# Kernel optimization log

Hardware: AMD Instinct MI355X
Metric: run time of the kernel (lower is better)

## Reference

```python
import jax, jax.numpy as jnp
import numpy as np

N_NODES = 100000
N_EDGES = 600000
HIDDEN = 128
LN_EPS = 1e-8


def setup_inputs() -> dict:
    key = jax.random.key(0)
    k1, k2, k3 = jax.random.split(key, 3)
    x = jax.random.normal(k1, (N_NODES, HIDDEN), dtype=jnp.float32)
    edge_index = jax.random.randint(k2, (2, N_EDGES), 0, N_NODES, dtype=jnp.int32)
    # GCNConv linear weight (glorot-ish scale) and bias
    W = jax.random.normal(k3, (HIDDEN, HIDDEN), dtype=jnp.float32) / np.sqrt(HIDDEN)
    b = jnp.zeros((HIDDEN,), dtype=jnp.float32)
    ln_gamma = jnp.ones((HIDDEN,), dtype=jnp.float32)
    ln_beta = jnp.zeros((HIDDEN,), dtype=jnp.float32)
    return {"x": x, "edge_index": edge_index, "W": W, "b": b,
            "ln_gamma": ln_gamma, "ln_beta": ln_beta}


def _gcn_layer(x, edge_index, W, b, ln_gamma, ln_beta):
    n = x.shape[0]
    # --- GCNConv (PyG semantics): add self-loops, sym-normalize, x@W, scatter ---
    loop = jnp.arange(n, dtype=edge_index.dtype)
    src = jnp.concatenate([edge_index[0], loop])  # [E+N]
    dst = jnp.concatenate([edge_index[1], loop])
    deg = jax.ops.segment_sum(jnp.ones_like(dst, dtype=x.dtype), dst,
                              num_segments=n)  # in-degree incl. self-loop
    dinv = jnp.where(deg > 0, jax.lax.rsqrt(deg), 0.0)
    norm = dinv[src] * dinv[dst]  # [E+N]
    h = x @ W  # [N, H]
    msg = h[src] * norm[:, None]  # gather + scale, [E+N, H]
    agg = jax.ops.segment_sum(msg, dst, num_segments=n) + b  # scatter-sum
    # --- ReLU -> (dropout = identity in eval) -> residual -> LayerNorm ---
    y = jax.nn.relu(agg) + x
    mu = jnp.mean(y, axis=-1, keepdims=True)
    var = jnp.mean(jnp.square(y - mu), axis=-1, keepdims=True)
    return (y - mu) * jax.lax.rsqrt(var + LN_EPS) * ln_gamma + ln_beta


def reference(x, edge_index, W, b, ln_gamma, ln_beta):
    return _gcn_layer(x, edge_index, W, b, ln_gamma, ln_beta)
```

## Files before the change

### kernel.cpp

```cpp
#include <hip/hip_runtime.h>

#define HID 128
#define CAP 32
#define BM 64
#define EUN 8

typedef unsigned short u16;
typedef unsigned int u32;
typedef __attribute__((ext_vector_type(8))) short short8v;
typedef __attribute__((ext_vector_type(4))) float f32x4;
typedef __attribute__((ext_vector_type(4))) u32 u32x4;

__device__ inline u16 f2bf(float f) {
    union { float f; u32 u; } c; c.f = f;
    u32 u = c.u;
    return (u16)((u + 0x7FFFu + ((u >> 16) & 1u)) >> 16);
}
__device__ inline u32 pack2(float lo, float hi) {
    return (u32)f2bf(lo) | ((u32)f2bf(hi) << 16);
}
__device__ inline float bflo(u32 u) {
    union { u32 u; float f; } c; c.u = u << 16; return c.f;
}
__device__ inline float bfhi(u32 u) {
    union { u32 u; float f; } c; c.u = u & 0xFFFF0000u; return c.f;
}
__device__ inline float bf2f(u16 b) {
    union { u32 u; float f; } c; c.u = ((u32)b) << 16; return c.f;
}

__global__ __launch_bounds__(256) void k_countfill(const int* __restrict__ src,
                                                   const int* __restrict__ dst,
                                                   int* __restrict__ cnt,
                                                   int* __restrict__ csr, int e) {
    const int base = blockIdx.x * (256 * EUN) + threadIdx.x;
    int d[EUN], s[EUN], slot[EUN];
    #pragma unroll
    for (int u = 0; u < EUN; ++u) {
        int i = base + u * 256;
        if (i < e) {
            d[u] = __builtin_nontemporal_load(&dst[i]);
            s[u] = __builtin_nontemporal_load(&src[i]);
        }
    }
    #pragma unroll
    for (int u = 0; u < EUN; ++u)
        if (base + u * 256 < e) slot[u] = atomicAdd(&cnt[d[u]], 1);
    #pragma unroll
    for (int u = 0; u < EUN; ++u)
        if (base + u * 256 < e && slot[u] < CAP)
            csr[(size_t)d[u] * CAP + slot[u]] = s[u];
}

__global__ __launch_bounds__(256) void k_prep(const float* __restrict__ x,
                                              u16* __restrict__ xbf,
                                              const float* __restrict__ W,
                                              u16* __restrict__ wswz, int n) {
    int t = blockIdx.x * blockDim.x + threadIdx.x;
    if (t < n * 16) {
        int g = t >> 4, l = t & 15;
        const float4* p = (const float4*)&x[(size_t)g * HID + l * 8];
        float4 v0 = p[0], v1 = p[1];
        uint4 o;
        o.x = pack2(v0.x, v0.y);
        o.y = pack2(v0.z, v0.w);
        o.z = pack2(v1.x, v1.y);
        o.w = pack2(v1.z, v1.w);
        *(uint4*)&xbf[(size_t)g * HID + l * 8] = o;
    }
    if (t < 128 * 128) {
        int i = t & 7;
        int lane = (t >> 3) & 63;
        int ct = (t >> 9) & 7;
        int ks = t >> 12;
        int k = ks * 32 + (lane >> 4) * 8 + i;
        int col = ct * 16 + (lane & 15);
        wswz[t] = f2bf(W[k * HID + col]);
    }
}

__global__ __launch_bounds__(256) void k_fused(const u16* __restrict__ xbf,
                                               const int* __restrict__ cnt,
                                               const int* __restrict__ csr,
                                               const u16* __restrict__ wswz,
                                               const float* __restrict__ bvec,
                                               const float* __restrict__ gamma,
                                               const float* __restrict__ beta,
                                               float* __restrict__ out, int n) {
    __shared__ uint4 lds4[1024];
    char* lds = (char*)lds4;
    const int tid = threadIdx.x;
    const int row0 = blockIdx.x * BM;

    {
        const int grp = tid >> 4;
        const int l16 = tid & 15;
        const int j8 = l16 * 8;
        #pragma unroll
        for (int k = 0; k < 4; ++k) {
            int r = grp * 4 + k;
            int g = row0 + r;
            uint4 pk = make_uint4(0, 0, 0, 0);
            if (g < n) {
                const int len = min(cnt[g], CAP);
                const float dd = rsqrtf((float)(cnt[g] + 1));
                float acc[8];
                {
                    float s2 = dd * dd;
                    u32x4 hv = *(const u32x4*)&xbf[(size_t)g * HID + j8];
                    acc[0] = bflo(hv.x) * s2; acc[1] = bfhi(hv.x) * s2;
                    acc[2] = bflo(hv.y) * s2; acc[3] = bfhi(hv.y) * s2;
                    acc[4] = bflo(hv.z) * s2; acc[5] = bfhi(hv.z) * s2;
                    acc[6] = bflo(hv.w) * s2; acc[7] = bfhi(hv.w) * s2;
                }
                const size_t off = (size_t)g * CAP;
                for (int base = 0; base < len; base += 16) {
                    int idx = base + l16;
                    int sk = csr[off + (idx < len ? idx : 0)];
                    float dv = (idx < len) ? rsqrtf((float)(cnt[sk] + 1)) : 0.f;
                    int mm = (min(16, len - base) + 3) & ~3;
                    for (int j = 0; j < mm; j += 4) {
                        int s0 = __shfl(sk, j + 0, 16);
                        int s1 = __shfl(sk, j + 1, 16);
                        int s2 = __shfl(sk, j + 2, 16);
                        int s3 = __shfl(sk, j + 3, 16);
                        float w0 = __shfl(dv, j + 0, 16) * dd;
                        float w1 = __shfl(dv, j + 1, 16) * dd;
                        float w2 = __shfl(dv, j + 2, 16) * dd;
                        float w3 = __shfl(dv, j + 3, 16) * dd;
                        u32x4 h0 = *(const u32x4*)&xbf[(size_t)s0 * HID + j8];
                        u32x4 h1 = *(const u32x4*)&xbf[(size_t)s1 * HID + j8];
                        u32x4 h2 = *(const u32x4*)&xbf[(size_t)s2 * HID + j8];
                        u32x4 h3 = *(const u32x4*)&xbf[(size_t)s3 * HID + j8];
                        acc[0] = fmaf(bflo(h0.x), w0, acc[0]); acc[1] = fmaf(bfhi(h0.x), w0, acc[1]);
                        acc[2] = fmaf(bflo(h0.y), w0, acc[2]); acc[3] = fmaf(bfhi(h0.y), w0, acc[3]);
                        acc[4] = fmaf(bflo(h0.z), w0, acc[4]); acc[5] = fmaf(bfhi(h0.z), w0, acc[5]);
                        acc[6] = fmaf(bflo(h0.w), w0, acc[6]); acc[7] = fmaf(bfhi(h0.w), w0, acc[7]);
                        acc[0] = fmaf(bflo(h1.x), w1, acc[0]); acc[1] = fmaf(bfhi(h1.x), w1, acc[1]);
                        acc[2] = fmaf(bflo(h1.y), w1, acc[2]); acc[3] = fmaf(bfhi(h1.y), w1, acc[3]);
                        acc[4] = fmaf(bflo(h1.z), w1, acc[4]); acc[5] = fmaf(bfhi(h1.z), w1, acc[5]);
                        acc[6] = fmaf(bflo(h1.w), w1, acc[6]); acc[7] = fmaf(bfhi(h1.w), w1, acc[7]);
                        acc[0] = fmaf(bflo(h2.x), w2, acc[0]); acc[1] = fmaf(bfhi(h2.x), w2, acc[1]);
                        acc[2] = fmaf(bflo(h2.y), w2, acc[2]); acc[3] = fmaf(bfhi(h2.y), w2, acc[3]);
                        acc[4] = fmaf(bflo(h2.z), w2, acc[4]); acc[5] = fmaf(bfhi(h2.z), w2, acc[5]);
                        acc[6] = fmaf(bflo(h2.w), w2, acc[6]); acc[7] = fmaf(bfhi(h2.w), w2, acc[7]);
                        acc[0] = fmaf(bflo(h3.x), w3, acc[0]); acc[1] = fmaf(bfhi(h3.x), w3, acc[1]);
                        acc[2] = fmaf(bflo(h3.y), w3, acc[2]); acc[3] = fmaf(bfhi(h3.y), w3, acc[3]);
                        acc[4] = fmaf(bflo(h3.z), w3, acc[4]); acc[5] = fmaf(bfhi(h3.z), w3, acc[5]);
                        acc[6] = fmaf(bflo(h3.w), w3, acc[6]); acc[7] = fmaf(bfhi(h3.w), w3, acc[7]);
                    }
                }
                pk.x = pack2(acc[0], acc[1]);
                pk.y = pack2(acc[2], acc[3]);
                pk.z = pack2(acc[4], acc[5]);
                pk.w = pack2(acc[6], acc[7]);
            }
            int byte = r * 256 + l16 * 16;
            byte ^= (r & 7) << 4;
            *(uint4*)(lds + byte) = pk;
        }
    }
    __syncthreads();

    const int w = tid >> 6;
    const int l = tid & 63;
    const int c15 = l & 15;
    const short8v* wfrag = (const short8v*)wswz;

    f32x4 acc[8];
    #pragma unroll
    for (int c = 0; c < 8; ++c) acc[c] = (f32x4){0.f, 0.f, 0.f, 0.f};

    #pragma unroll
    for (int ks = 0; ks < 4; ++ks) {
        int row = w * 16 + c15;
        int byte = row * 256 + ks * 64 + (l >> 4) * 16;
        byte ^= (row & 7) << 4;
        short8v a = *(const short8v*)(lds + byte);
        #pragma unroll
        for (int ct = 0; ct < 8; ++ct) {
            short8v b = wfrag[(ks * 8 + ct) * 64 + l];
            acc[ct] = __builtin_amdgcn_mfma_f32_16x16x32_bf16(a, b, acc[ct], 0, 0, 0);
        }
    }

    float bb[8], gg[8], bz[8];
    #pragma unroll
    for (int ct = 0; ct < 8; ++ct) {
        bb[ct] = bvec[ct * 16 + c15];
        gg[ct] = gamma[ct * 16 + c15];
        bz[ct] = beta[ct * 16 + c15];
    }
    #pragma unroll
    for (int j = 0; j < 4; ++j) {
        int gr = row0 + w * 16 + (l >> 4) * 4 + j;
        if (gr < n) {
            const u16* xr = xbf + (size_t)gr * HID + c15;
            float v[8];
            #pragma unroll
            for (int ct = 0; ct < 8; ++ct)
                v[ct] = fmaxf(acc[ct][j] + bb[ct], 0.f) + bf2f(xr[ct * 16]);
            float sum = 0.f;
            #pragma unroll
            for (int ct = 0; ct < 8; ++ct) sum += v[ct];
            #pragma unroll
            for (int o = 1; o < 16; o <<= 1) sum += __shfl_xor(sum, o, 16);
            float mu = sum * (1.0f / HID);
            float d[8], vs = 0.f;
            #pragma unroll
            for (int ct = 0; ct < 8; ++ct) { d[ct] = v[ct] - mu; vs = fmaf(d[ct], d[ct], vs); }
            #pragma unroll
            for (int o = 1; o < 16; o <<= 1) vs += __shfl_xor(vs, o, 16);
            float inv = rsqrtf(vs * (1.0f / HID) + 1e-8f);
            float* orow = out + (size_t)gr * HID + c15;
            #pragma unroll
            for (int ct = 0; ct < 8; ++ct)
                __builtin_nontemporal_store(fmaf(d[ct] * inv, gg[ct], bz[ct]), &orow[ct * 16]);
        }
    }
}

extern "C" void kernel_launch(void* const* d_in, const int* in_sizes, int n_in,
                              void* d_out, int out_size, void* d_ws, size_t ws_size,
                              hipStream_t stream) {
    const float* x     = (const float*)d_in[0];
    const int*   ei    = (const int*)d_in[1];
    const float* W     = (const float*)d_in[2];
    const float* b     = (const float*)d_in[3];
    const float* gamma = (const float*)d_in[4];
    const float* beta  = (const float*)d_in[5];
    float* out = (float*)d_out;

    const int n = in_sizes[0] / HID;
    const int e = in_sizes[1] / 2;
    const int* src = ei;
    const int* dst = ei + e;

    u16* xbf  = (u16*)d_ws;
    int* cnt  = (int*)(xbf + (size_t)n * HID);
    int* csr  = cnt + n;
    u16* wswz = (u16*)(csr + (size_t)n * CAP);

    hipMemsetAsync(cnt, 0, (size_t)n * sizeof(int), stream);
    k_countfill<<<(e + 256 * EUN - 1) / (256 * EUN), 256, 0, stream>>>(src, dst, cnt, csr, e);
    k_prep<<<((size_t)n * 16 + 255) / 256, 256, 0, stream>>>(x, xbf, W, wswz, n);
    k_fused<<<(n + BM - 1) / BM, 256, 0, stream>>>(
        xbf, cnt, csr, wswz, b, gamma, beta, out, n);
}
```

Measured before the change: 102.3 us.

## Gather neighbor features as pre-scaled FP8 rows instead of bf16

The prep kernel now also writes a copy of x in FP8, with each row already scaled by its source-side degree normalisation, plus a zeroed sentinel row at index n. The aggregation loop gathers 128-byte FP8 rows instead of 256-byte bf16 rows. It no longer needs the per-neighbour count load and rsqrt, and it applies the destination scale once at the end. This halves the bandwidth of the random-access gather, at the cost of FP8 quantisation error in the aggregated messages.

```diff
diff --git a/kernel.cpp b/kernel.cpp
--- a/kernel.cpp
+++ b/kernel.cpp
@@ -8,6 +8,7 @@
 typedef unsigned short u16;
 typedef unsigned int u32;
 typedef __attribute__((ext_vector_type(8))) short short8v;
+typedef __attribute__((ext_vector_type(2))) float f32x2;
 typedef __attribute__((ext_vector_type(4))) float f32x4;
 typedef __attribute__((ext_vector_type(4))) u32 u32x4;
 
@@ -54,6 +55,8 @@
 
 __global__ __launch_bounds__(256) void k_prep(const float* __restrict__ x,
                                               u16* __restrict__ xbf,
+                                              u32* __restrict__ x8,
+                                              const int* __restrict__ cnt,
                                               const float* __restrict__ W,
                                               u16* __restrict__ wswz, int n) {
     int t = blockIdx.x * blockDim.x + threadIdx.x;
@@ -67,6 +70,12 @@
         o.z = pack2(v1.x, v1.y);
         o.w = pack2(v1.z, v1.w);
         *(uint4*)&xbf[(size_t)g * HID + l * 8] = o;
+        float dd = rsqrtf((float)(cnt[g] + 1));
+        u32 a = (u32)__builtin_amdgcn_cvt_pk_fp8_f32(v0.x * dd, v0.y * dd, 0, false);
+        a = (u32)__builtin_amdgcn_cvt_pk_fp8_f32(v0.z * dd, v0.w * dd, a, true);
+        u32 bq = (u32)__builtin_amdgcn_cvt_pk_fp8_f32(v1.x * dd, v1.y * dd, 0, false);
+        bq = (u32)__builtin_amdgcn_cvt_pk_fp8_f32(v1.z * dd, v1.w * dd, bq, true);
+        *(uint2*)&x8[(size_t)g * 32 + l * 2] = make_uint2(a, bq);
     }
     if (t < 128 * 128) {
         int i = t & 7;
@@ -80,6 +89,7 @@
 }
 
 __global__ __launch_bounds__(256) void k_fused(const u16* __restrict__ xbf,
+                                               const u32* __restrict__ x8,
                                                const int* __restrict__ cnt,
                                                const int* __restrict__ csr,
                                                const u16* __restrict__ wswz,
@@ -104,56 +114,62 @@
             if (g < n) {
                 const int len = min(cnt[g], CAP);
                 const float dd = rsqrtf((float)(cnt[g] + 1));
-                float acc[8];
-                {
-                    float s2 = dd * dd;
-                    u32x4 hv = *(const u32x4*)&xbf[(size_t)g * HID + j8];
-                    acc[0] = bflo(hv.x) * s2; acc[1] = bfhi(hv.x) * s2;
-                    acc[2] = bflo(hv.y) * s2; acc[3] = bfhi(hv.y) * s2;
-                    acc[4] = bflo(hv.z) * s2; acc[5] = bfhi(hv.z) * s2;
-                    acc[6] = bflo(hv.w) * s2; acc[7] = bfhi(hv.w) * s2;
-                }
+                float sum[8] = {0.f, 0.f, 0.f, 0.f, 0.f, 0.f, 0.f, 0.f};
                 const size_t off = (size_t)g * CAP;
                 for (int base = 0; base < len; base += 16) {
                     int idx = base + l16;
-                    int sk = csr[off + (idx < len ? idx : 0)];
-                    float dv = (idx < len) ? rsqrtf((float)(cnt[sk] + 1)) : 0.f;
+                    int sk = (idx < len) ? csr[off + idx] : n;
                     int mm = (min(16, len - base) + 3) & ~3;
                     for (int j = 0; j < mm; j += 4) {
                         int s0 = __shfl(sk, j + 0, 16);
                         int s1 = __shfl(sk, j + 1, 16);
                         int s2 = __shfl(sk, j + 2, 16);
                         int s3 = __shfl(sk, j + 3, 16);
-                        float w0 = __shfl(dv, j + 0, 16) * dd;
-                        float w1 = __shfl(dv, j + 1, 16) * dd;
-                        float w2 = __shfl(dv, j + 2, 16) * dd;
-                        float w3 = __shfl(dv, j + 3, 16) * dd;
-                        u32x4 h0 = *(const u32x4*)&xbf[(size_t)s0 * HID + j8];
-                        u32x4 h1 = *(const u32x4*)&xbf[(size_t)s1 * HID + j8];
-                        u32x4 h2 = *(const u32x4*)&xbf[(size_t)s2 * HID + j8];
-                        u32x4 h3 = *(const u32x4*)&xbf[(size_t)s3 * HID + j8];
-                        acc[0] = fmaf(bflo(h0.x), w0, acc[0]); acc[1] = fmaf(bfhi(h0.x), w0, acc[1]);
-                        acc[2] = fmaf(bflo(h0.y), w0, acc[2]); acc[3] = fmaf(bfhi(h0.y), w0, acc[3]);
-                        acc[4] = fmaf(bflo(h0.z), w0, acc[4]); acc[5] = fmaf(bfhi(h0.z), w0, acc[5]);
-                        acc[6] = fmaf(bflo(h0.w), w0, acc[6]); acc[7] = fmaf(bfhi(h0.w), w0, acc[7]);
-                        acc[0] = fmaf(bflo(h1.x), w1, acc[0]); acc[1] = fmaf(bfhi(h1.x), w1, acc[1]);
-                        acc[2] = fmaf(bflo(h1.y), w1, acc[2]); acc[3] = fmaf(bfhi(h1.y), w1, acc[3]);
-                        acc[4] = fmaf(bflo(h1.z), w1, acc[4]); acc[5] = fmaf(bfhi(h1.z), w1, acc[5]);
-                        acc[6] = fmaf(bflo(h1.w), w1, acc[6]); acc[7] = fmaf(bfhi(h1.w), w1, acc[7]);
-                        acc[0] = fmaf(bflo(h2.x), w2, acc[0]); acc[1] = fmaf(bfhi(h2.x), w2, acc[1]);
-                        acc[2] = fmaf(bflo(h2.y), w2, acc[2]); acc[3] = fmaf(bfhi(h2.y), w2, acc[3]);
-                        acc[4] = fmaf(bflo(h2.z), w2, acc[4]); acc[5] = fmaf(bfhi(h2.z), w2, acc[5]);
-                        acc[6] = fmaf(bflo(h2.w), w2, acc[6]); acc[7] = fmaf(bfhi(h2.w), w2, acc[7]);
-                        acc[0] = fmaf(bflo(h3.x), w3, acc[0]); acc[1] = fmaf(bfhi(h3.x), w3, acc[1]);
-                        acc[2] = fmaf(bflo(h3.y), w3, acc[2]); acc[3] = fmaf(bfhi(h3.y), w3, acc[3]);
-                        acc[4] = fmaf(bflo(h3.z), w3, acc[4]); acc[5] = fmaf(bfhi(h3.z), w3, acc[5]);
-                        acc[6] = fmaf(bflo(h3.w), w3, acc[6]); acc[7] = fmaf(bfhi(h3.w), w3, acc[7]);
+                        uint2 h0 = *(const uint2*)&x8[(size_t)s0 * 32 + l16 * 2];
+                        uint2 h1 = *(const uint2*)&x8[(size_t)s1 * 32 + l16 * 2];
+                        uint2 h2 = *(const uint2*)&x8[(size_t)s2 * 32 + l16 * 2];
+                        uint2 h3 = *(const uint2*)&x8[(size_t)s3 * 32 + l16 * 2];
+                        f32x2 p0, p1, p2, p3;
+                        p0 = __builtin_amdgcn_cvt_pk_f32_fp8(h0.x, false);
+                        p1 = __builtin_amdgcn_cvt_pk_f32_fp8(h0.x, true);
+                        p2 = __builtin_amdgcn_cvt_pk_f32_fp8(h0.y, false);
+                        p3 = __builtin_amdgcn_cvt_pk_f32_fp8(h0.y, true);
+                        sum[0] += p0.x; sum[1] += p0.y; sum[2] += p1.x; sum[3] += p1.y;
+                        sum[4] += p2.x; sum[5] += p2.y; sum[6] += p3.x; sum[7] += p3.y;
+                        p0 = __builtin_amdgcn_cvt_pk_f32_fp8(h1.x, false);
+                        p1 = __builtin_amdgcn_cvt_pk_f32_fp8(h1.x, true);
+                        p2 = __builtin_amdgcn_cvt_pk_f32_fp8(h1.y, false);
+                        p3 = __builtin_amdgcn_cvt_pk_f32_fp8(h1.y, true);
+                        sum[0] += p0.x; sum[1] += p0.y; sum[2] += p1.x; sum[3] += p1.y;
+                        sum[4] += p2.x; sum[5] += p2.y; sum[6] += p3.x; sum[7] += p3.y;
+                        p0 = __builtin_amdgcn_cvt_pk_f32_fp8(h2.x, false);
+                        p1 = __builtin_amdgcn_cvt_pk_f32_fp8(h2.x, true);
+                        p2 = __builtin_amdgcn_cvt_pk_f32_fp8(h2.y, false);
+                        p3 = __builtin_amdgcn_cvt_pk_f32_fp8(h2.y, true);
+                        sum[0] += p0.x; sum[1] += p0.y; sum[2] += p1.x; sum[3] += p1.y;
+                        sum[4] += p2.x; sum[5] += p2.y; sum[6] += p3.x; sum[7] += p3.y;
+                        p0 = __builtin_amdgcn_cvt_pk_f32_fp8(h3.x, false);
+                        p1 = __builtin_amdgcn_cvt_pk_f32_fp8(h3.x, true);
+                        p2 = __builtin_amdgcn_cvt_pk_f32_fp8(h3.y, false);
+                        p3 = __builtin_amdgcn_cvt_pk_f32_fp8(h3.y, true);
+                        sum[0] += p0.x; sum[1] += p0.y; sum[2] += p1.x; sum[3] += p1.y;
+                        sum[4] += p2.x; sum[5] += p2.y; sum[6] += p3.x; sum[7] += p3.y;
                     }
                 }
-                pk.x = pack2(acc[0], acc[1]);
-                pk.y = pack2(acc[2], acc[3]);
-                pk.z = pack2(acc[4], acc[5]);
-                pk.w = pack2(acc[6], acc[7]);
+                float dd2 = dd * dd;
+                u32x4 hv = *(const u32x4*)&xbf[(size_t)g * HID + j8];
+                float a0 = fmaf(sum[0], dd, bflo(hv.x) * dd2);
+                float a1 = fmaf(sum[1], dd, bfhi(hv.x) * dd2);
+                float a2 = fmaf(sum[2], dd, bflo(hv.y) * dd2);
+                float a3 = fmaf(sum[3], dd, bfhi(hv.y) * dd2);
+                float a4 = fmaf(sum[4], dd, bflo(hv.z) * dd2);
+                float a5 = fmaf(sum[5], dd, bfhi(hv.z) * dd2);
+                float a6 = fmaf(sum[6], dd, bflo(hv.w) * dd2);
+                float a7 = fmaf(sum[7], dd, bfhi(hv.w) * dd2);
+                pk.x = pack2(a0, a1);
+                pk.y = pack2(a2, a3);
+                pk.z = pack2(a4, a5);
+                pk.w = pack2(a6, a7);
             }
             int byte = r * 256 + l16 * 16;
             byte ^= (r & 7) << 4;
@@ -237,13 +253,14 @@
     const int* dst = ei + e;
 
     u16* xbf  = (u16*)d_ws;
-    int* cnt  = (int*)(xbf + (size_t)n * HID);
+    u32* x8   = (u32*)(xbf + (size_t)n * HID);
+    int* cnt  = (int*)(x8 + ((size_t)n + 1) * 32);
     int* csr  = cnt + n;
     u16* wswz = (u16*)(csr + (size_t)n * CAP);
 
-    hipMemsetAsync(cnt, 0, (size_t)n * sizeof(int), stream);
+    hipMemsetAsync(x8 + (size_t)n * 32, 0, 128 + (size_t)n * sizeof(int), stream);
     k_countfill<<<(e + 256 * EUN - 1) / (256 * EUN), 256, 0, stream>>>(src, dst, cnt, csr, e);
-    k_prep<<<((size_t)n * 16 + 255) / 256, 256, 0, stream>>>(x, xbf, W, wswz, n);
+    k_prep<<<((size_t)n * 16 + 255) / 256, 256, 0, stream>>>(x, xbf, x8, cnt, W, wswz, n);
     k_fused<<<(n + BM - 1) / BM, 256, 0, stream>>>(
-        xbf, cnt, csr, wswz, b, gamma, beta, out, n);
-}
+        xbf, x8, cnt, csr, wswz, b, gamma, beta, out, n);
+}
```

Result: faster. 96.91 us (median of 2 runs) (-5.3%).
